# Performance work log

Measured on AMD Instinct MI355X. Metric: run time of the kernel, lower is better.

## Reference

```python
import jax, jax.numpy as jnp
import numpy as np

B, C, T, H, W, L = 4, 256, 8, 16, 16, 8
NO = 8                # num_offsets
D = C // NO           # per-head feature dim for offset/weight MLPs
EPS = 1e-5


def setup_inputs() -> dict:
    key = jax.random.key(0)
    ks = jax.random.split(key, 6)
    return {
        "features": jax.random.normal(ks[0], (B, C, T, H, W, L), jnp.float32),
        "pos": jax.random.normal(ks[1], (B, C, T, H, W, L), jnp.float32),
        "Wp": jax.random.normal(ks[2], (C, 3 * C), jnp.float32) * 0.02,  # 1x1x1 conv: 3C -> C
        "bp": jnp.zeros((C,), jnp.float32),
        "Wo": jax.random.normal(ks[3], (D, 3), jnp.float32) * 0.02,      # offset_embed Linear(d,3)
        "bo": jnp.zeros((3,), jnp.float32),
        "Ww": jax.random.normal(ks[4], (D, 2), jnp.float32) * 0.02,      # weight_embed Linear(d,2)
        "bw": jnp.zeros((2,), jnp.float32),
    }


def _trilinear_sample(feat, coords):
    """feat: (N,C,D1,D2,D3); coords: (N,G,3) in [-1,1] (axis order D1,D2,D3).
    align_corners=False, zeros padding (matches F.grid_sample semantics)."""
    N, Cc, D1, D2, D3 = feat.shape
    sizes = jnp.asarray([D1, D2, D3], feat.dtype)
    pix = ((coords + 1.0) * sizes - 1.0) * 0.5       # unnormalize to pixel coords
    lo = jnp.floor(pix)
    frac = pix - lo                                   # (N,G,3)
    lo = lo.astype(jnp.int32)
    dims = jnp.asarray([D1, D2, D3], jnp.int32)
    feat_flat = feat.reshape(N, Cc, D1 * D2 * D3)
    out = jnp.zeros((N, Cc, coords.shape[1]), feat.dtype)
    for dz in (0, 1):
        for dy in (0, 1):
            for dx in (0, 1):
                off = jnp.asarray([dz, dy, dx], jnp.int32)
                idx = lo + off                        # (N,G,3)
                wz = jnp.where(dz, frac[..., 0], 1.0 - frac[..., 0])
                wy = jnp.where(dy, frac[..., 1], 1.0 - frac[..., 1])
                wx = jnp.where(dx, frac[..., 2], 1.0 - frac[..., 2])
                wgt = wz * wy * wx                    # (N,G)
                valid = jnp.all((idx >= 0) & (idx < dims), axis=-1)
                idc = jnp.clip(idx, 0, dims - 1)
                lin = (idc[..., 0] * D2 + idc[..., 1]) * D3 + idc[..., 2]  # (N,G)
                vals = jnp.take_along_axis(feat_flat, lin[:, None, :], axis=2)  # (N,C,G)
                out = out + vals * (wgt * valid)[:, None, :]
    return out


def reference(features, pos, Wp, bp, Wo, bo, Ww, bw):
    Bv, Cv, Tv, Hv, Wv, Lv = features.shape
    BT = Bv * Tv
    feat = features.transpose(0, 2, 1, 3, 4, 5).reshape(BT, Cv, Hv, Wv, Lv)
    posr = pos.transpose(0, 2, 1, 3, 4, 5).reshape(BT, Cv, Hv, Wv, Lv)
    # global context + projection (1x1x1 conv over 3C channels) + ReLU
    glob = feat.mean(axis=(2, 3, 4), keepdims=True)
    src = jnp.concatenate([feat, posr, jnp.broadcast_to(glob, feat.shape)], axis=1)  # (BT,3C,H,W,L)
    proj = jax.nn.relu(jnp.einsum('nixyz,oi->noxyz', src, Wp) + bp[None, :, None, None, None])
    osrc = proj.transpose(0, 2, 3, 4, 1).reshape(BT, Hv, Wv, Lv, NO, D)
    # per-voxel per-head offsets in (0,1) and scalar weights
    offset = jax.nn.sigmoid(osrc @ Wo + bo)                      # (BT,H,W,L,NO,3)
    wgt = jax.nn.softmax(osrc @ Ww + bw, axis=-1)[..., 1]        # (BT,H,W,L,NO)
    # base flow field in [-1,1], deform in logit space, re-sigmoid
    base = jnp.stack(jnp.meshgrid(jnp.linspace(-1.0, 1.0, Hv),
                                  jnp.linspace(-1.0, 1.0, Wv),
                                  jnp.linspace(-1.0, 1.0, Lv), indexing='ij'), axis=-1)
    base01 = jnp.clip((base + 1.0) * 0.5, EPS, 1.0 - EPS)
    logit = jnp.log(base01 / (1.0 - base01))                     # (H,W,L,3)
    sp = jax.nn.sigmoid(logit[None, :, :, :, None, :] + offset)  # (BT,H,W,L,NO,3)
    grid = (sp * 2.0 - 1.0).transpose(0, 4, 1, 2, 3, 5).reshape(BT, NO * Hv * Wv * Lv, 3)
    sampled = _trilinear_sample(feat, grid).reshape(BT, Cv, NO, Hv, Wv, Lv)
    out = feat + jnp.einsum('bcnhwl,bhwln->bchwl', sampled, wgt)
    return out.reshape(Bv, Tv, Cv, Hv, Wv, Lv).transpose(0, 2, 1, 3, 4, 5)
```

## Files before the change

kernel.cpp:

```cpp
#include <hip/hip_runtime.h>

#define BB 4
#define CC 256
#define TT 8
#define HH 16
#define WW 16
#define LL 8
#define NO 8
#define DD 32
#define BT 32
#define VV 2048
#define KIN 512
#define EPS_ 1e-5f

typedef short bf16x8 __attribute__((ext_vector_type(8)));
typedef float f32x4 __attribute__((ext_vector_type(4)));
typedef float f32x2 __attribute__((ext_vector_type(2)));

static __device__ __forceinline__ float b2f(unsigned short u) {
    return __uint_as_float(((unsigned int)u) << 16);
}
static __device__ __forceinline__ float b2f_lo(unsigned int x) {
    return __uint_as_float(x << 16);
}
static __device__ __forceinline__ float b2f_hi(unsigned int x) {
    return __uint_as_float(x & 0xffff0000u);
}
static __device__ __forceinline__ unsigned short f2b(float f) {
    unsigned int x = __float_as_uint(f);
    unsigned int r = x + 0x7fffu + ((x >> 16) & 1u);
    return (unsigned short)(r >> 16);
}
static __device__ __forceinline__ unsigned int f2b_pk(float lo, float hi) {
    return (unsigned int)f2b(lo) | ((unsigned int)f2b(hi) << 16);
}
static __device__ __forceinline__ float sigm(float x) {
    return 1.0f / (1.0f + __expf(-x));
}
static __device__ __forceinline__ void glds16(const void* g, void* l) {
    __builtin_amdgcn_global_load_lds(
        (const __attribute__((address_space(1))) void*)g,
        (__attribute__((address_space(3))) void*)l, 16, 0, 0);
}
static __device__ __forceinline__ int xsw(int x, int j) {
    switch (j) {
        case 1:  return __builtin_amdgcn_update_dpp(0, x, 0xB1, 0xF, 0xF, true);
        case 2:  return __builtin_amdgcn_update_dpp(0, x, 0x4E, 0xF, 0xF, true);
        case 8:  return __builtin_amdgcn_update_dpp(0, x, 0x128, 0xF, 0xF, true);
        case 4:  return __builtin_amdgcn_ds_swizzle(x, 0x101F);
        case 16: return __builtin_amdgcn_ds_swizzle(x, 0x401F);
        default: return __shfl_xor(x, 32);
    }
}

__global__ __launch_bounds__(256) void k0_prep(const float* __restrict__ Wp,
                                               unsigned short* __restrict__ Wa) {
    int i = blockIdx.x * 256 + threadIdx.x;
    int o = i >> 9, k = i & 511;
    Wa[i] = f2b(Wp[o * 768 + k]);
}

__global__ __launch_bounds__(256) void k1_transpose(const float* __restrict__ features,
                                                    const float* __restrict__ pos,
                                                    unsigned short* __restrict__ srcT,
                                                    float* __restrict__ gpart) {
    const int vt  = blockIdx.x;
    const int ch  = blockIdx.y & 1;
    const int arr = blockIdx.y >> 1;
    const int n   = blockIdx.z;
    const int v0 = vt * 128;
    const int b = n >> 3, t = n & 7;
    const int tid = threadIdx.x;
    const int w = tid >> 6;
    const int lane = tid & 63;
    const int v16 = lane >> 2;
    const int cs  = lane & 3;

    __shared__ uint2 sg[128 * 33];

    const float* src = arr ? pos : features;
    const size_t cb = ((size_t)(b * CC + ch * 128 + w * 32) * TT + t) * (size_t)VV
                      + v0 + v16 * 4;

    float4 f[2][4][2];
    #pragma unroll
    for (int i = 0; i < 2; ++i)
        #pragma unroll
        for (int e = 0; e < 4; ++e)
            #pragma unroll
            for (int vh = 0; vh < 2; ++vh)
                f[i][e][vh] = *(const float4*)(src + cb
                                + (size_t)(i * 16 + cs * 4 + e) * (TT * VV) + vh * 64);

    #pragma unroll
    for (int i = 0; i < 2; ++i) {
        const int cq = w * 8 + i * 4 + cs;
        #pragma unroll
        for (int vh = 0; vh < 2; ++vh) {
            #pragma unroll
            for (int k = 0; k < 4; ++k) {
                const int v = vh * 64 + v16 * 4 + k;
                uint2 u;
                u.x = f2b_pk(((const float*)&f[i][0][vh])[k], ((const float*)&f[i][1][vh])[k]);
                u.y = f2b_pk(((const float*)&f[i][2][vh])[k], ((const float*)&f[i][3][vh])[k]);
                sg[v * 33 + cq] = u;
            }
        }
    }

    if (arr == 0) {
        float part[2][4];
        #pragma unroll
        for (int i = 0; i < 2; ++i)
            #pragma unroll
            for (int e = 0; e < 4; ++e) {
                part[i][e] = f[i][e][0].x + f[i][e][0].y + f[i][e][0].z + f[i][e][0].w
                           + f[i][e][1].x + f[i][e][1].y + f[i][e][1].z + f[i][e][1].w;
                #pragma unroll
                for (int m = 4; m < 64; m <<= 1)
                    part[i][e] += __shfl_xor(part[i][e], m);
            }
        if (lane < 4) {
            float* gp = gpart + ((size_t)n * 16 + vt) * CC + ch * 128 + w * 32 + cs * 4;
            *(float4*)gp        = make_float4(part[0][0], part[0][1], part[0][2], part[0][3]);
            *(float4*)(gp + 16) = make_float4(part[1][0], part[1][1], part[1][2], part[1][3]);
        }
    }
    __syncthreads();

    const int vh2 = tid >> 4;
    const int q   = tid & 15;
    unsigned short* ob = srcT + ((size_t)n * VV + v0) * KIN + arr * 256 + ch * 128 + q * 8;
    #pragma unroll
    for (int j = 0; j < 8; ++j) {
        const int v = j * 16 + vh2;
        uint2 lo = sg[v * 33 + q * 2];
        uint2 hi = sg[v * 33 + q * 2 + 1];
        uint4 o;
        o.x = lo.x; o.y = lo.y; o.z = hi.x; o.w = hi.y;
        *(uint4*)(ob + (size_t)v * KIN) = o;
    }
}

__global__ __launch_bounds__(256) void k2_gterm(const float* __restrict__ gpart,
                                                const float* __restrict__ Wp,
                                                const float* __restrict__ bp,
                                                float* __restrict__ gterm) {
    const int n = blockIdx.x;
    const int o = threadIdx.x;
    __shared__ float gl[CC];
    float s = 0.0f;
    const float* gp = gpart + (size_t)n * 16 * CC + o;
    #pragma unroll 8
    for (int vt = 0; vt < 16; ++vt) s += gp[vt * CC];
    gl[o] = s * (1.0f / (float)VV);
    __syncthreads();
    const float4* wrow = (const float4*)(Wp + (size_t)o * 768 + 512);
    const float4* g4 = (const float4*)gl;
    float acc = bp[o];
    #pragma unroll 8
    for (int c = 0; c < 64; ++c) {
        float4 w = wrow[c], g = g4[c];
        acc += w.x * g.x + w.y * g.y + w.z * g.z + w.w * g.w;
    }
    gterm[n * CC + o] = acc;
}

__global__ __launch_bounds__(256) void k3_gemm(const unsigned short* __restrict__ Wa,
                                               const unsigned short* __restrict__ srcT,
                                               const float* __restrict__ gterm,
                                               unsigned short* __restrict__ projT) {
    const int n  = blockIdx.x;
    const int mb = blockIdx.y;
    const int nb = blockIdx.z;
    const int tid = threadIdx.x;
    const int m0 = mb * 128, v0 = nb * 128;

    __shared__ short As[128 * 32];
    __shared__ short Bs[128 * 32];

    const int w = tid >> 6;
    const int lane = tid & 63;
    const int wm = w >> 1, wn = w & 1;
    const int lr = lane & 15, lq = lane >> 4;

    f32x4 acc[4][4];
    #pragma unroll
    for (int i = 0; i < 4; ++i)
        #pragma unroll
        for (int j = 0; j < 4; ++j)
            acc[i][j] = (f32x4){0.f, 0.f, 0.f, 0.f};

    const int rsub = lane >> 2;
    const int ksub = (lane & 3) * 8;
    const unsigned short* agp = Wa   + (size_t)(m0 + w * 16 + rsub) * KIN + ksub;
    const unsigned short* bgp = srcT + ((size_t)n * VV + v0 + w * 16 + rsub) * KIN + ksub;
    short* alds0 = &As[(w * 16) * 32];
    short* alds1 = &As[(64 + w * 16) * 32];
    short* blds0 = &Bs[(w * 16) * 32];
    short* blds1 = &Bs[(64 + w * 16) * 32];

    for (int k0 = 0; k0 < KIN; k0 += 32) {
        __syncthreads();
        glds16(agp + k0,                    alds0);
        glds16(agp + k0 + (size_t)64 * KIN, alds1);
        glds16(bgp + k0,                    blds0);
        glds16(bgp + k0 + (size_t)64 * KIN, blds1);
        __syncthreads();

        bf16x8 af[4], bf[4];
        #pragma unroll
        for (int i = 0; i < 4; ++i)
            af[i] = *(const bf16x8*)&As[(wm * 64 + i * 16 + lr) * 32 + lq * 8];
        #pragma unroll
        for (int j = 0; j < 4; ++j)
            bf[j] = *(const bf16x8*)&Bs[(wn * 64 + j * 16 + lr) * 32 + lq * 8];
        #pragma unroll
        for (int i = 0; i < 4; ++i)
            #pragma unroll
            for (int j = 0; j < 4; ++j)
                acc[i][j] = __builtin_amdgcn_mfma_f32_16x16x32_bf16(af[i], bf[j], acc[i][j], 0, 0, 0);
    }

    #pragma unroll
    for (int i = 0; i < 4; ++i) {
        const int og = m0 + wm * 64 + i * 16 + lq * 4;
        float4 g = *(const float4*)(gterm + n * CC + og);
        #pragma unroll
        for (int j = 0; j < 4; ++j) {
            const int vg = v0 + wn * 64 + j * 16 + lr;
            float x0 = fmaxf(acc[i][j][0] + g.x, 0.0f);
            float x1 = fmaxf(acc[i][j][1] + g.y, 0.0f);
            float x2 = fmaxf(acc[i][j][2] + g.z, 0.0f);
            float x3 = fmaxf(acc[i][j][3] + g.w, 0.0f);
            ushort4 st;
            st.x = f2b(x0); st.y = f2b(x1); st.z = f2b(x2); st.w = f2b(x3);
            *(ushort4*)&projT[((size_t)n * VV + vg) * CC + og] = st;
        }
    }
}

__global__ __launch_bounds__(256) void k5_fused(const unsigned short* __restrict__ projT,
                                                const unsigned short* __restrict__ srcT,
                                                const float* __restrict__ Wo,
                                                const float* __restrict__ bo,
                                                const float* __restrict__ Ww,
                                                const float* __restrict__ bw,
                                                unsigned short* __restrict__ res) {
    __shared__ float sWo[96], sWd[32], sb[5];
    __shared__ int   sK[4 * 64];
    __shared__ float sW[4 * 64];
    const int tid = threadIdx.x;
    const int wid = tid >> 6;
    const int lane = tid & 63;
    if (tid < 96) sWo[tid] = Wo[tid];
    if (tid < 32) sWd[tid] = Ww[2 * tid + 1] - Ww[2 * tid];
    if (tid < 3)  sb[tid] = bo[tid];
    if (tid < 2)  sb[3 + tid] = bw[tid];
    __syncthreads();

    const int gv = blockIdx.x * 4 + wid;
    const int n = gv >> 11;
    const int v = gv & 2047;

    const int hd = lane >> 3;
    const int s  = lane & 7;

    uint2 pr = *(const uint2*)(projT + ((size_t)n * VV + v) * CC + lane * 4);
    float t0 = b2f_lo(pr.x), t1 = b2f_hi(pr.x), t2 = b2f_lo(pr.y), t3 = b2f_hi(pr.y);
    const int d0 = s * 4;
    float o0 = t0 * sWo[3 * d0 + 0] + t1 * sWo[3 * d0 + 3] + t2 * sWo[3 * d0 + 6] + t3 * sWo[3 * d0 + 9];
    float o1 = t0 * sWo[3 * d0 + 1] + t1 * sWo[3 * d0 + 4] + t2 * sWo[3 * d0 + 7] + t3 * sWo[3 * d0 + 10];
    float o2 = t0 * sWo[3 * d0 + 2] + t1 * sWo[3 * d0 + 5] + t2 * sWo[3 * d0 + 8] + t3 * sWo[3 * d0 + 11];
    float zw = t0 * sWd[d0] + t1 * sWd[d0 + 1] + t2 * sWd[d0 + 2] + t3 * sWd[d0 + 3];
    #pragma unroll
    for (int m = 1; m < 8; m <<= 1) {
        o0 += __shfl_xor(o0, m);
        o1 += __shfl_xor(o1, m);
        o2 += __shfl_xor(o2, m);
        zw += __shfl_xor(zw, m);
    }
    o0 += sb[0]; o1 += sb[1]; o2 += sb[2];
    const float wgt = sigm(zw + sb[4] - sb[3]);

    const int h = v >> 7, wv_ = (v >> 3) & 15, l = v & 7;
    float ph = fminf(fmaxf(h   * (1.0f / 15.0f), EPS_), 1.0f - EPS_);
    float pw = fminf(fmaxf(wv_ * (1.0f / 15.0f), EPS_), 1.0f - EPS_);
    float pl = fminf(fmaxf(l   * (1.0f / 7.0f),  EPS_), 1.0f - EPS_);
    float sph = sigm(__logf(ph / (1.0f - ph)) + sigm(o0));
    float spw = sigm(__logf(pw / (1.0f - pw)) + sigm(o1));
    float spl = sigm(__logf(pl / (1.0f - pl)) + sigm(o2));
    float pixh = sph * 16.0f - 0.5f;
    float pixw = spw * 16.0f - 0.5f;
    float pixl = spl * 8.0f  - 0.5f;
    float flh = floorf(pixh), flw = floorf(pixw), fll = floorf(pixl);
    float fh = pixh - flh, fw = pixw - flw, fl = pixl - fll;
    const int dz = s >> 2, dy = (s >> 1) & 1, dx = s & 1;
    int iz = (int)flh + dz, iy = (int)flw + dy, ix = (int)fll + dx;
    float wt = (dz ? fh : 1.0f - fh) * (dy ? fw : 1.0f - fw) * (dx ? fl : 1.0f - fl) * wgt;
    bool valid = ((unsigned)iz < 16u) && ((unsigned)iy < 16u) && ((unsigned)ix < 8u);
    int key = valid ? (((iz * 16 + iy) * 8 + ix) << 10) : 0;
    float w = valid ? wt : 0.0f;

    #pragma unroll
    for (int k = 2; k <= 64; k <<= 1) {
        #pragma unroll
        for (int j = k >> 1; j > 0; j >>= 1) {
            int pk = xsw(key, j);
            float pw2 = __int_as_float(xsw(__float_as_int(w), j));
            bool keepMin = (((lane & k) == 0) == ((lane & j) == 0));
            bool take = keepMin ? (pk < key) : (pk > key);
            if (take) { key = pk; w = pw2; }
        }
    }
    #pragma unroll
    for (int d = 1; d < 64; d <<= 1) {
        float tw = __shfl_up(w, d);
        int   tk = __shfl_up(key, d);
        if (lane >= d && tk == key) w += tw;
    }
    int nk = __shfl_down(key, 1);
    bool tail = (lane == 63) || (nk != key);
    unsigned long long mask = __ballot(tail);
    int cnt = __popcll(mask);
    int cidx = __popcll(mask & ((1ull << lane) - 1ull));

    sK[wid * 64 + lane] = 0;
    sW[wid * 64 + lane] = 0.0f;
    __syncthreads();
    if (tail) { sK[wid * 64 + cidx] = key; sW[wid * 64 + cidx] = w; }
    __syncthreads();
    int ck = sK[wid * 64 + lane];
    float cw = sW[wid * 64 + lane];

    const char* slabB = (const char*)srcT + (size_t)n * VV * KIN * 2 + lane * 8;
    f32x2 a01 = (f32x2){0.f, 0.f}, a23 = (f32x2){0.f, 0.f};
    const int iters = (cnt + 7) & ~7;
    #pragma unroll 1
    for (int e = 0; e < iters; e += 8) {
        uint2 f[8]; float wvv[8];
        #pragma unroll
        for (int u = 0; u < 8; ++u) {
            int rk = __builtin_amdgcn_readlane(ck, e + u);
            wvv[u] = __uint_as_float(
                        __builtin_amdgcn_readlane(__float_as_uint(cw), e + u));
            f[u] = *(const uint2*)(slabB + (unsigned)rk);
        }
        #pragma unroll
        for (int u = 0; u < 8; ++u) {
            a01 += wvv[u] * (f32x2){b2f_lo(f[u].x), b2f_hi(f[u].x)};
            a23 += wvv[u] * (f32x2){b2f_lo(f[u].y), b2f_hi(f[u].y)};
        }
    }

    uint2 st;
    st.x = f2b_pk(a01.x, a01.y);
    st.y = f2b_pk(a23.x, a23.y);
    *(uint2*)&res[((size_t)n * VV + v) * CC + lane * 4] = st;
}

__global__ __launch_bounds__(256) void k6_final(const float* __restrict__ features,
                                                const unsigned short* __restrict__ res,
                                                float* __restrict__ out) {
    const int n = blockIdx.x;
    const int c0 = blockIdx.y * 128;
    const int v0 = blockIdx.z * 64;
    const int b = n >> 3, t = n & 7;
    const int tid = threadIdx.x;

    __shared__ uint2 t6[64 * 33];

    const int lr = tid >> 5;
    const int cp = tid & 31;
    #pragma unroll
    for (int p = 0; p < 8; ++p) {
        const int r = p * 8 + lr;
        t6[r * 33 + cp] = *(const uint2*)&res[((size_t)n * VV + v0 + r) * CC + c0 + cp * 4];
    }
    __syncthreads();

    const unsigned short* t6s = (const unsigned short*)t6;
    const int tx = tid & 63;
    const int cl0 = tid >> 6;
    #pragma unroll 8
    for (int p = 0; p < 32; ++p) {
        const int cl = p * 4 + cl0;
        const int c = c0 + cl;
        size_t oidx = (((size_t)b * CC + c) * TT + t) * VV + v0 + tx;
        unsigned short val = t6s[(tx * 33 + (cl >> 2)) * 4 + (cl & 3)];
        out[oidx] = features[oidx] + b2f(val);
    }
}

extern "C" void kernel_launch(void* const* d_in, const int* in_sizes, int n_in,
                              void* d_out, int out_size, void* d_ws, size_t ws_size,
                              hipStream_t stream) {
    (void)in_sizes; (void)n_in; (void)out_size; (void)ws_size;
    const float* features = (const float*)d_in[0];
    const float* pos      = (const float*)d_in[1];
    const float* Wp       = (const float*)d_in[2];
    const float* bp       = (const float*)d_in[3];
    const float* Wo       = (const float*)d_in[4];
    const float* bo       = (const float*)d_in[5];
    const float* Ww       = (const float*)d_in[6];
    const float* bw       = (const float*)d_in[7];
    float* out = (float*)d_out;

    char* ws = (char*)d_ws;
    unsigned short* srcT  = (unsigned short*)ws;
    unsigned short* Wa    = (unsigned short*)(ws + 67108864);
    float*          gterm = (float*)(ws + 67403776);
    unsigned short* projT = (unsigned short*)(ws + 67436544);
    float*          gpart = (float*)(ws + 100990976);
    unsigned short* res   = projT;

    k0_prep<<<512, 256, 0, stream>>>(Wp, Wa);
    k1_transpose<<<dim3(16, 4, 32), 256, 0, stream>>>(features, pos, srcT, gpart);
    k2_gterm<<<32, 256, 0, stream>>>(gpart, Wp, bp, gterm);
    k3_gemm<<<dim3(32, 2, 16), 256, 0, stream>>>(Wa, srcT, gterm, projT);
    k5_fused<<<16384, 256, 0, stream>>>(projT, srcT, Wo, bo, Ww, bw, res);
    k6_final<<<dim3(32, 2, 32), 256, 0, stream>>>(features, res, out);
}
```

Measured before the change: 318.5 us.

## Widen GEMM tile to full M with 512 threads; sort lane indices instead of weights

The projection GEMM now uses 512-thread blocks that each cover all 256 output channels for a 128-voxel tile. Each srcT tile is therefore loaded once instead of twice, halving redundant B loads at the cost of fewer, larger blocks and more LDS. In the sampling kernel, the bitonic sort now sorts a combined key holding the lane id and gathers the weight once with a shuffle afterwards. This drops one cross-lane exchange per sort step.

```diff
diff --git a/kernel.cpp b/kernel.cpp
--- a/kernel.cpp
+++ b/kernel.cpp
@@ -166,22 +166,22 @@
     gterm[n * CC + o] = acc;
 }
 
-__global__ __launch_bounds__(256) void k3_gemm(const unsigned short* __restrict__ Wa,
+__global__ __launch_bounds__(512) void k3_gemm(const unsigned short* __restrict__ Wa,
                                                const unsigned short* __restrict__ srcT,
                                                const float* __restrict__ gterm,
                                                unsigned short* __restrict__ projT) {
     const int n  = blockIdx.x;
-    const int mb = blockIdx.y;
-    const int nb = blockIdx.z;
+    const int nb = blockIdx.y;
     const int tid = threadIdx.x;
-    const int m0 = mb * 128, v0 = nb * 128;
-
-    __shared__ short As[128 * 32];
+    const int v0 = nb * 128;
+
+    __shared__ short As[256 * 32];
     __shared__ short Bs[128 * 32];
 
     const int w = tid >> 6;
     const int lane = tid & 63;
-    const int wm = w >> 1, wn = w & 1;
+    const int wm = w >> 1;
+    const int wn = w & 1;
     const int lr = lane & 15, lq = lane >> 4;
 
     f32x4 acc[4][4];
@@ -193,19 +193,17 @@
 
     const int rsub = lane >> 2;
     const int ksub = (lane & 3) * 8;
-    const unsigned short* agp = Wa   + (size_t)(m0 + w * 16 + rsub) * KIN + ksub;
+    const unsigned short* agp = Wa   + (size_t)(w * 16 + rsub) * KIN + ksub;
     const unsigned short* bgp = srcT + ((size_t)n * VV + v0 + w * 16 + rsub) * KIN + ksub;
     short* alds0 = &As[(w * 16) * 32];
-    short* alds1 = &As[(64 + w * 16) * 32];
-    short* blds0 = &Bs[(w * 16) * 32];
-    short* blds1 = &Bs[(64 + w * 16) * 32];
+    short* alds1 = &As[(128 + w * 16) * 32];
+    short* blds  = &Bs[(w * 16) * 32];
 
     for (int k0 = 0; k0 < KIN; k0 += 32) {
         __syncthreads();
-        glds16(agp + k0,                    alds0);
-        glds16(agp + k0 + (size_t)64 * KIN, alds1);
-        glds16(bgp + k0,                    blds0);
-        glds16(bgp + k0 + (size_t)64 * KIN, blds1);
+        glds16(agp + k0,                     alds0);
+        glds16(agp + k0 + (size_t)128 * KIN, alds1);
+        glds16(bgp + k0,                     blds);
         __syncthreads();
 
         bf16x8 af[4], bf[4];
@@ -224,7 +222,7 @@
 
     #pragma unroll
     for (int i = 0; i < 4; ++i) {
-        const int og = m0 + wm * 64 + i * 16 + lq * 4;
+        const int og = wm * 64 + i * 16 + lq * 4;
         float4 g = *(const float4*)(gterm + n * CC + og);
         #pragma unroll
         for (int j = 0; j < 4; ++j) {
@@ -299,28 +297,31 @@
     int iz = (int)flh + dz, iy = (int)flw + dy, ix = (int)fll + dx;
     float wt = (dz ? fh : 1.0f - fh) * (dy ? fw : 1.0f - fw) * (dx ? fl : 1.0f - fl) * wgt;
     bool valid = ((unsigned)iz < 16u) && ((unsigned)iy < 16u) && ((unsigned)ix < 8u);
-    int key = valid ? (((iz * 16 + iy) * 8 + ix) << 10) : 0;
-    float w = valid ? wt : 0.0f;
-
+    int lin = valid ? ((iz * 16 + iy) * 8 + ix) : 0;
+    float w0 = valid ? wt : 0.0f;
+
+    int key2 = (lin << 6) | lane;
     #pragma unroll
     for (int k = 2; k <= 64; k <<= 1) {
         #pragma unroll
         for (int j = k >> 1; j > 0; j >>= 1) {
-            int pk = xsw(key, j);
-            float pw2 = __int_as_float(xsw(__float_as_int(w), j));
+            int pk = xsw(key2, j);
             bool keepMin = (((lane & k) == 0) == ((lane & j) == 0));
-            bool take = keepMin ? (pk < key) : (pk > key);
-            if (take) { key = pk; w = pw2; }
-        }
-    }
+            bool take = keepMin ? (pk < key2) : (pk > key2);
+            if (take) key2 = pk;
+        }
+    }
+    float w = __shfl(w0, key2 & 63);
+    int klin = key2 >> 6;
+
     #pragma unroll
     for (int d = 1; d < 64; d <<= 1) {
         float tw = __shfl_up(w, d);
-        int   tk = __shfl_up(key, d);
-        if (lane >= d && tk == key) w += tw;
-    }
-    int nk = __shfl_down(key, 1);
-    bool tail = (lane == 63) || (nk != key);
+        int   tk = __shfl_up(klin, d);
+        if (lane >= d && tk == klin) w += tw;
+    }
+    int nk = __shfl_down(klin, 1);
+    bool tail = (lane == 63) || (nk != klin);
     unsigned long long mask = __ballot(tail);
     int cnt = __popcll(mask);
     int cidx = __popcll(mask & ((1ull << lane) - 1ull));
@@ -328,7 +329,7 @@
     sK[wid * 64 + lane] = 0;
     sW[wid * 64 + lane] = 0.0f;
     __syncthreads();
-    if (tail) { sK[wid * 64 + cidx] = key; sW[wid * 64 + cidx] = w; }
+    if (tail) { sK[wid * 64 + cidx] = klin << 10; sW[wid * 64 + cidx] = w; }
     __syncthreads();
     int ck = sK[wid * 64 + lane];
     float cw = sW[wid * 64 + lane];
@@ -417,7 +418,7 @@
     k0_prep<<<512, 256, 0, stream>>>(Wp, Wa);
     k1_transpose<<<dim3(16, 4, 32), 256, 0, stream>>>(features, pos, srcT, gpart);
     k2_gterm<<<32, 256, 0, stream>>>(gpart, Wp, bp, gterm);
-    k3_gemm<<<dim3(32, 2, 16), 256, 0, stream>>>(Wa, srcT, gterm, projT);
+    k3_gemm<<<dim3(32, 16), 512, 0, stream>>>(Wa, srcT, gterm, projT);
     k5_fused<<<16384, 256, 0, stream>>>(projT, srcT, Wo, bo, Ww, bw, res);
     k6_final<<<dim3(32, 2, 32), 256, 0, stream>>>(features, res, out);
 }
```

Measured after the change: 312.8 us. About the same (-1.8%).
